# Kernel optimization log

Hardware: AMD Instinct MI355X
Metric: run time of the kernel (lower is better)

Reference implementation:

```python
import jax, jax.numpy as jnp
import numpy as np


def gru_layer(x, h0, Wih, Whh, bih, bhh):
    """Run a single-direction PyTorch-style GRU over x: [B,T,D] -> ([B,T,H], [B,H]).
    Gate order matches torch (r, z, n)."""
    xg = jnp.einsum('btd,gd->btg', x, Wih) + bih  # precompute input gates [B,T,3H]

    def step(h, gi):
        gh = h @ Whh.T + bhh
        ir, iz, inn = jnp.split(gi, 3, axis=-1)
        hr, hz, hn = jnp.split(gh, 3, axis=-1)
        r = jax.nn.sigmoid(ir + hr)
        z = jax.nn.sigmoid(iz + hz)
        n = jnp.tanh(inn + r * hn)
        h_new = (1.0 - z) * n + z * h
        return h_new, h_new

    hT, ys = jax.lax.scan(step, h0, jnp.swapaxes(xg, 0, 1))
    return jnp.swapaxes(ys, 0, 1), hT


def setup_inputs() -> dict:
    key = jax.random.key(0)
    ks = jax.random.split(key, 13)
    B, T, D, H = 64, 100, 75, 1024
    s = 0.02
    rn = lambda k, shp: (jax.random.normal(k, shp, jnp.float32) * s)
    return {
        'input_tensor': jax.random.normal(ks[0], (B, T, D), jnp.float32),
        'seq_len': jax.random.randint(ks[1], (B,), 1, T + 1, jnp.int32),
        'enc_Wih0': rn(ks[2], (2, 3 * H, D)),
        'enc_Whh0': rn(ks[3], (2, 3 * H, H)),
        'enc_b0': rn(ks[4], (2, 2, 3 * H)),
        'enc_Wih': rn(ks[5], (2, 2, 3 * H, 2 * H)),
        'enc_Whh': rn(ks[6], (2, 2, 3 * H, H)),
        'enc_b': rn(ks[7], (2, 2, 2, 3 * H)),
        'dec_Wih': rn(ks[8], (6 * H, D)),
        'dec_Whh': rn(ks[9], (6 * H, 2 * H)),
        'dec_b': rn(ks[10], (2, 6 * H)),
        'out_W': rn(ks[11], (D, 2 * H)),
        'out_b': rn(ks[12], (D,)),
    }


def reference(input_tensor, seq_len, enc_Wih0, enc_Whh0, enc_b0,
              enc_Wih, enc_Whh, enc_b, dec_Wih, dec_Whh, dec_b,
              out_W, out_b):
    B, T, D = input_tensor.shape
    H = enc_Whh0.shape[-1]
    h0 = jnp.zeros((B, H), input_tensor.dtype)

    # Encoder: the original feeds the bidirectional GRU one timestep at a time,
    # so BOTH direction parameter sets run left-to-right (degenerate bidir).
    yf, _ = gru_layer(input_tensor, h0, enc_Wih0[0], enc_Whh0[0], enc_b0[0, 0], enc_b0[0, 1])
    yb, _ = gru_layer(input_tensor, h0, enc_Wih0[1], enc_Whh0[1], enc_b0[1, 0], enc_b0[1, 1])
    y = jnp.concatenate([yf, yb], axis=-1)  # [B,T,2H]
    for l in range(enc_Wih.shape[0]):  # layers 1..num_layers-1
        yf, _ = gru_layer(y, h0, enc_Wih[l, 0], enc_Whh[l, 0], enc_b[l, 0, 0], enc_b[l, 0, 1])
        yb, _ = gru_layer(y, h0, enc_Wih[l, 1], enc_Whh[l, 1], enc_b[l, 1, 0], enc_b[l, 1, 1])
        y = jnp.concatenate([yf, yb], axis=-1)

    sl = jnp.clip(seq_len, 1, T)
    enc_hidden = y[jnp.arange(B), sl - 1][None]  # (1, B, 2H): last valid step per sample

    # Decoder: 1-layer GRU (hidden 2H) over a zeros input sequence, init = enc_hidden
    de_in = jnp.zeros_like(input_tensor)
    ys, _ = gru_layer(de_in, enc_hidden[0], dec_Wih, dec_Whh, dec_b[0], dec_b[1])
    dec_out = ys @ out_W.T + out_b  # [B,T,D]
    return (enc_hidden, dec_out)
```

## Files before the change

### kernel.cpp

```cpp
#include <hip/hip_runtime.h>
#include <math.h>

typedef unsigned short u16;
typedef unsigned long long u64;
typedef __attribute__((ext_vector_type(8))) short s16x8;
typedef __attribute__((ext_vector_type(4))) short s16x4;
typedef __attribute__((ext_vector_type(4))) float f4v;

__device__ __forceinline__ float bf2f(short u) {
    union { unsigned int i; float f; } v;
    v.i = ((unsigned int)(u16)u) << 16;
    return v.f;
}
__device__ __forceinline__ u16 f2bf(float f) {
    union { float f; unsigned int i; } v; v.f = f;
    unsigned int x = v.i;
    return (u16)((x + 0x7FFFu + ((x >> 16) & 1u)) >> 16);
}

__device__ __forceinline__ u64 coh_load_u64(const u16* p) {
    return __hip_atomic_load((const u64*)p, __ATOMIC_RELAXED, __HIP_MEMORY_SCOPE_AGENT);
}
__device__ __forceinline__ void coh_store_u64(u16* p, u64 v) {
    __hip_atomic_store((u64*)p, v, __ATOMIC_RELAXED, __HIP_MEMORY_SCOPE_AGENT);
}

__device__ __forceinline__ void flag_barrier(unsigned* slot, int nblk, unsigned tgt) {
    __syncthreads();
    if (threadIdx.x == 0)
        __hip_atomic_store(&slot[blockIdx.x], tgt, __ATOMIC_RELAXED, __HIP_MEMORY_SCOPE_AGENT);
    if (blockIdx.x == 0 && (int)threadIdx.x < 64) {
        int spins = 0;
        for (;;) {
            int ok = 1;
            for (int i = (int)threadIdx.x; i < nblk; i += 64)
                ok &= (__hip_atomic_load(&slot[i], __ATOMIC_RELAXED,
                                         __HIP_MEMORY_SCOPE_AGENT) >= tgt);
            if (__all(ok)) break;
            __builtin_amdgcn_s_sleep(2);
            if (++spins > (1 << 20)) break;
        }
        if (threadIdx.x == 0)
            __hip_atomic_store(&slot[192], tgt, __ATOMIC_RELAXED, __HIP_MEMORY_SCOPE_AGENT);
    }
    if (threadIdx.x == 0) {
        int spins2 = 0;
        while (__hip_atomic_load(&slot[192], __ATOMIC_RELAXED, __HIP_MEMORY_SCOPE_AGENT) < tgt) {
            __builtin_amdgcn_s_sleep(1);
            if (++spins2 > (1 << 20)) break;
        }
    }
    __syncthreads();
    asm volatile("" ::: "memory");
}

__global__ void zero_bar(unsigned* p, int n) {
    int i = blockIdx.x * blockDim.x + threadIdx.x;
    if (i < n) p[i] = 0;
}

__global__ __launch_bounds__(256)
void cvt_bf16v(const float* __restrict__ src, u16* __restrict__ dst, int n4) {
    int i = blockIdx.x * 256 + threadIdx.x;
    int stride = gridDim.x * 256;
    for (; i < n4; i += stride) {
        f4v v = ((const f4v*)src)[i];
        s16x4 o;
#pragma unroll
        for (int j = 0; j < 4; ++j) o[j] = (short)f2bf(v[j]);
        ((s16x4*)dst)[i] = o;
    }
}

__global__ __launch_bounds__(256)
void cvt_pack(const float* __restrict__ src, u16* __restrict__ dst,
              int JT, int KB, int K)
{
    int fid = blockIdx.x * 4 + (threadIdx.x >> 6);
    int lane = threadIdx.x & 63;
    int nf = 3 * JT * KB;
    if (fid >= nf) return;
    int g = fid / (JT * KB);
    int rem = fid - g * JT * KB;
    int jt = rem / KB;
    int kb = rem - jt * KB;
    int j = jt * 16 + (lane & 15);
    int k = kb * 32 + (lane >> 4) * 8;
    const float* s = src + ((size_t)g * JT * 16 + j) * K + k;
    f4v a = *(const f4v*)s;
    f4v b = *(const f4v*)(s + 4);
    s16x8 o;
#pragma unroll
    for (int i = 0; i < 4; ++i) { o[i] = (short)f2bf(a[i]); o[4 + i] = (short)f2bf(b[i]); }
    *(s16x8*)(dst + (size_t)fid * 512 + lane * 8) = o;
}

__global__ __launch_bounds__(256)
void xg0_kernel(const float* __restrict__ x,
                const float* __restrict__ W,
                const float* __restrict__ bih,
                u16* __restrict__ xg)
{
    const int bt0 = blockIdx.x * 16;
    __shared__ float xl[16][76];
    for (int idx = threadIdx.x; idx < 16 * 75; idx += 256) {
        int r = idx / 75, k = idx % 75;
        xl[r][k] = x[(size_t)(bt0 + r) * 75 + k];
    }
    __syncthreads();
    for (int i = 0; i < 12; ++i) {
        int g = threadIdx.x + i * 256;
        const float* wr = W + (size_t)g * 75;
        float bv = bih[g];
        float acc[16];
#pragma unroll
        for (int r = 0; r < 16; ++r) acc[r] = bv;
        for (int k = 0; k < 75; ++k) {
            float w = wr[k];
#pragma unroll
            for (int r = 0; r < 16; ++r) acc[r] += xl[r][k] * w;
        }
#pragma unroll
        for (int r = 0; r < 16; ++r)
            xg[(size_t)(bt0 + r) * 3072 + g] = f2bf(acc[r]);
    }
}

__global__ __launch_bounds__(256)
void xg_gemm(const u16* __restrict__ A, const float* __restrict__ Bm,
             const float* __restrict__ bias, u16* __restrict__ C, int K)
{
    __shared__ u16 Alds[64 * 40];
    __shared__ u16 Blds[64 * 40];
    const int m0 = blockIdx.x * 64;
    const int n0 = blockIdx.y * 64;
    const int wave = threadIdx.x >> 6;
    const int lane = threadIdx.x & 63;
    const int r = threadIdx.x >> 2;
    const int kk = (threadIdx.x & 3) * 8;
    const int mrow = wave * 16 + (lane & 15);
    const int kq = (lane >> 4) * 8;
    f4v acc[4];
#pragma unroll
    for (int nt = 0; nt < 4; ++nt) acc[nt] = (f4v){0.f, 0.f, 0.f, 0.f};

    for (int k0 = 0; k0 < K; k0 += 32) {
        *(s16x8*)&Alds[r * 40 + kk] = *(const s16x8*)(A + (size_t)(m0 + r) * K + k0 + kk);
        f4v b0v = *(const f4v*)(Bm + (size_t)(n0 + r) * K + k0 + kk);
        f4v b1v = *(const f4v*)(Bm + (size_t)(n0 + r) * K + k0 + kk + 4);
        s16x8 bb;
#pragma unroll
        for (int i = 0; i < 4; ++i) { bb[i] = (short)f2bf(b0v[i]); bb[4 + i] = (short)f2bf(b1v[i]); }
        *(s16x8*)&Blds[r * 40 + kk] = bb;
        __syncthreads();
        s16x8 a = *(const s16x8*)&Alds[mrow * 40 + kq];
#pragma unroll
        for (int nt = 0; nt < 4; ++nt) {
            s16x8 b = *(const s16x8*)&Blds[(nt * 16 + (lane & 15)) * 40 + kq];
            acc[nt] = __builtin_amdgcn_mfma_f32_16x16x32_bf16(a, b, acc[nt], 0, 0, 0);
        }
        __syncthreads();
    }
    const int col = lane & 15;
    const int rq = (lane >> 4) * 4;
#pragma unroll
    for (int nt = 0; nt < 4; ++nt) {
        int n = n0 + nt * 16 + col;
        float bbv = bias[n];
#pragma unroll
        for (int rg = 0; rg < 4; ++rg) {
            int m = m0 + wave * 16 + rq + rg;
            C[(size_t)m * 3072 + n] = f2bf(acc[nt][rg] + bbv);
        }
    }
}

__global__ __launch_bounds__(256)
void enc_persist(const u16* __restrict__ Wp,
                 const float* __restrict__ bias,
                 const u16* __restrict__ xg,
                 u16* __restrict__ hbf,
                 u16* __restrict__ y,
                 int dir, unsigned* __restrict__ bar)
{
    __shared__ u16 Al[16 * 1024];
    __shared__ u16 OutE[16 * 64];
    const int tid = threadIdx.x;
    const int lane = tid & 63;
    const int wv = tid >> 6;
    const int xcd = blockIdx.x & 7;
    const int jg = xcd * 2 + ((blockIdx.x >> 3) & 1);
    const int b0 = (blockIdx.x >> 4) * 16;
    const int jc = jg * 64 + wv * 16 + (lane & 15);
    const int jt = jg * 4 + wv;
    const int kq = (lane >> 4) * 8;
    const int arow = lane & 15;
    const int axor = (arow & 7) << 3;
    const float bhr = bias[3072 + jc];
    const float bhz = bias[4096 + jc];
    const float bhn = bias[5120 + jc];
    const u16* pR = Wp + ((size_t)(0 * 64 + jt) * 32) * 512 + lane * 8;
    const u16* pZ = Wp + ((size_t)(1 * 64 + jt) * 32) * 512 + lane * 8;
    const u16* pN = Wp + ((size_t)(2 * 64 + jt) * 32) * 512 + lane * 8;
    const int brow = b0 + (lane >> 4) * 4;
    f4v hold = {0.f, 0.f, 0.f, 0.f};

    for (int t = 0; t < 100; ++t) {
        f4v aR = {0.f, 0.f, 0.f, 0.f}, aZ = aR, aN = aR;
        if (t > 0) {
            const u16* hb = hbf + (size_t)(t & 1) * 65536 + (size_t)b0 * 1024;
            u64 tmp[16];
#pragma unroll
            for (int g = 0; g < 8; ++g) {
                int c = tid + g * 256;
                const u16* gp = hb + (size_t)(c >> 7) * 1024 + (c & 127) * 8;
                tmp[2 * g]     = coh_load_u64(gp);
                tmp[2 * g + 1] = coh_load_u64(gp + 4);
            }
#pragma unroll
            for (int g = 0; g < 8; ++g) {
                int c = tid + g * 256;
                int di = (c * 8) ^ (((c >> 7) & 7) << 3);
                *(u64*)&Al[di]     = tmp[2 * g];
                *(u64*)&Al[di + 4] = tmp[2 * g + 1];
            }
            __syncthreads();
            const int abase = arow * 1024 + kq;
            s16x8 cR = *(const s16x8*)(pR);
            s16x8 cZ = *(const s16x8*)(pZ);
            s16x8 cN = *(const s16x8*)(pN);
            for (int kb = 0; kb < 32; ++kb) {
                int kn = (kb + 1 < 32) ? kb + 1 : kb;
                s16x8 nR = *(const s16x8*)(pR + (size_t)kn * 512);
                s16x8 nZ = *(const s16x8*)(pZ + (size_t)kn * 512);
                s16x8 nN = *(const s16x8*)(pN + (size_t)kn * 512);
                s16x8 av = *(const s16x8*)&Al[(abase + kb * 32) ^ axor];
                aR = __builtin_amdgcn_mfma_f32_16x16x32_bf16(av, cR, aR, 0, 0, 0);
                aZ = __builtin_amdgcn_mfma_f32_16x16x32_bf16(av, cZ, aZ, 0, 0, 0);
                aN = __builtin_amdgcn_mfma_f32_16x16x32_bf16(av, cN, aN, 0, 0, 0);
                cR = nR; cZ = nZ; cN = nN;
            }
        }
#pragma unroll
        for (int r = 0; r < 4; ++r) {
            int b = brow + r;
            const u16* xr = xg + ((size_t)b * 100 + t) * 3072;
            float pr = bf2f((short)xr[jc]) + aR[r] + bhr;
            float pz = bf2f((short)xr[1024 + jc]) + aZ[r] + bhz;
            float pn = bf2f((short)xr[2048 + jc]);
            float rg = 1.f / (1.f + expf(-pr));
            float zg = 1.f / (1.f + expf(-pz));
            float ng = tanhf(pn + rg * (aN[r] + bhn));
            float hnew = (1.f - zg) * ng + zg * hold[r];
            hold[r] = hnew;
            OutE[((lane >> 4) * 4 + r) * 64 + wv * 16 + (lane & 15)] = f2bf(hnew);
        }
        __syncthreads();
        if (tid < 128) {
            int bl = tid >> 3, jl = (tid & 7) * 8;
            s16x8 v = *(const s16x8*)&OutE[bl * 64 + jl];
            const u64* pv = (const u64*)&v;
            u16* hw = hbf + (size_t)((t + 1) & 1) * 65536
                    + (size_t)(b0 + bl) * 1024 + jg * 64 + jl;
            coh_store_u64(hw, pv[0]);
            coh_store_u64(hw + 4, pv[1]);
            *(s16x8*)(y + ((size_t)(b0 + bl) * 100 + t) * 2048
                        + (size_t)dir * 1024 + jg * 64 + jl) = v;
        }
        if (t < 99) flag_barrier(bar, 64, (unsigned)(t + 1));
    }
}

__global__ __launch_bounds__(256)
void dec_persist(const u16* __restrict__ Wp,
                 const float* __restrict__ db,
                 const float* __restrict__ h32,
                 u16* __restrict__ hbf,
                 u16* __restrict__ ys,
                 unsigned* __restrict__ bar)
{
    __shared__ u16 Al[16 * 2048];
    __shared__ u16 OutD[16 * 64];
    const int tid = threadIdx.x;
    const int lane = tid & 63;
    const int wv = tid >> 6;
    const int xcd = blockIdx.x & 7;
    const int idx = blockIdx.x >> 3;
    const int jg = xcd * 4 + (idx & 3);
    const int b0 = (idx >> 2) * 16;
    const int jc = jg * 64 + wv * 16 + (lane & 15);
    const int jt = jg * 4 + wv;
    const int kq = (lane >> 4) * 8;
    const int arow = lane & 15;
    const int axor = (arow & 7) << 3;
    const float gir = db[jc]        + db[6144 + jc];
    const float giz = db[2048 + jc] + db[8192 + jc];
    const float gin = db[4096 + jc];
    const float bhn = db[10240 + jc];
    const u16* pR = Wp + ((size_t)(0 * 128 + jt) * 64) * 512 + lane * 8;
    const u16* pZ = Wp + ((size_t)(1 * 128 + jt) * 64) * 512 + lane * 8;
    const u16* pN = Wp + ((size_t)(2 * 128 + jt) * 64) * 512 + lane * 8;
    f4v hold;
#pragma unroll
    for (int r = 0; r < 4; ++r)
        hold[r] = h32[(size_t)(b0 + (lane >> 4) * 4 + r) * 2048 + jc];

    for (int t = 0; t < 100; ++t) {
        const u16* hb = hbf + (size_t)(t & 1) * 131072 + (size_t)b0 * 2048;
#pragma unroll
        for (int h = 0; h < 2; ++h) {
            u64 tmp[16];
#pragma unroll
            for (int g = 0; g < 8; ++g) {
                int c = tid + (h * 8 + g) * 256;
                const u16* gp = hb + (size_t)(c >> 8) * 2048 + (c & 255) * 8;
                tmp[2 * g]     = coh_load_u64(gp);
                tmp[2 * g + 1] = coh_load_u64(gp + 4);
            }
#pragma unroll
            for (int g = 0; g < 8; ++g) {
                int c = tid + (h * 8 + g) * 256;
                int di = (c * 8) ^ (((c >> 8) & 7) << 3);
                *(u64*)&Al[di]     = tmp[2 * g];
                *(u64*)&Al[di + 4] = tmp[2 * g + 1];
            }
        }
        __syncthreads();
        f4v aR = {0.f, 0.f, 0.f, 0.f}, aZ = aR, aN = aR;
        const int abase = arow * 2048 + kq;
        s16x8 cR = *(const s16x8*)(pR);
        s16x8 cZ = *(const s16x8*)(pZ);
        s16x8 cN = *(const s16x8*)(pN);
        for (int kb = 0; kb < 64; ++kb) {
            int kn = (kb + 1 < 64) ? kb + 1 : kb;
            s16x8 nR = *(const s16x8*)(pR + (size_t)kn * 512);
            s16x8 nZ = *(const s16x8*)(pZ + (size_t)kn * 512);
            s16x8 nN = *(const s16x8*)(pN + (size_t)kn * 512);
            s16x8 av = *(const s16x8*)&Al[(abase + kb * 32) ^ axor];
            aR = __builtin_amdgcn_mfma_f32_16x16x32_bf16(av, cR, aR, 0, 0, 0);
            aZ = __builtin_amdgcn_mfma_f32_16x16x32_bf16(av, cZ, aZ, 0, 0, 0);
            aN = __builtin_amdgcn_mfma_f32_16x16x32_bf16(av, cN, aN, 0, 0, 0);
            cR = nR; cZ = nZ; cN = nN;
        }
        __syncthreads();
#pragma unroll
        for (int r = 0; r < 4; ++r) {
            float pr = gir + aR[r];
            float pz = giz + aZ[r];
            float rg = 1.f / (1.f + expf(-pr));
            float zg = 1.f / (1.f + expf(-pz));
            float ng = tanhf(gin + rg * (aN[r] + bhn));
            float hnew = (1.f - zg) * ng + zg * hold[r];
            hold[r] = hnew;
            OutD[((lane >> 4) * 4 + r) * 64 + wv * 16 + (lane & 15)] = f2bf(hnew);
        }
        __syncthreads();
        if (tid < 128) {
            int bl = tid >> 3, jl = (tid & 7) * 8;
            s16x8 v = *(const s16x8*)&OutD[bl * 64 + jl];
            const u64* pv = (const u64*)&v;
            u16* hw = hbf + (size_t)((t + 1) & 1) * 131072
                    + (size_t)(b0 + bl) * 2048 + jg * 64 + jl;
            coh_store_u64(hw, pv[0]);
            coh_store_u64(hw + 4, pv[1]);
            *(s16x8*)(ys + ((size_t)(b0 + bl) * 100 + t) * 2048 + jg * 64 + jl) = v;
        }
        if (t < 99) flag_barrier(bar, 128, (unsigned)(t + 1));
    }
}

__global__ __launch_bounds__(256)
void gather_kernel(const int* __restrict__ seq_len, const u16* __restrict__ y,
                   float* __restrict__ out_enc, float* __restrict__ h32d,
                   u16* __restrict__ hbfd)
{
    int idx = blockIdx.x * 256 + threadIdx.x;
    int b = idx >> 11, j = idx & 2047;
    int s = seq_len[b];
    s = s < 1 ? 1 : (s > 100 ? 100 : s);
    u16 v = y[((size_t)b * 100 + (s - 1)) * 2048 + j];
    float f = bf2f((short)v);
    out_enc[idx] = f;
    h32d[idx] = f;
    hbfd[idx] = v;
}

__global__ __launch_bounds__(256)
void proj_kernel(const u16* __restrict__ ys, const float* __restrict__ oW,
                 const float* __restrict__ oB, float* __restrict__ dec_out)
{
    const int r0 = blockIdx.x * 8;
    __shared__ float yl[8][2048];
    __shared__ float psum[3][8][76];
    for (int idx = threadIdx.x; idx < 2048; idx += 256) {
        int rr = idx >> 8, cc = idx & 255;
        s16x8 v = ((const s16x8*)(ys + (size_t)(r0 + rr) * 2048))[cc];
#pragma unroll
        for (int i = 0; i < 8; ++i) yl[rr][cc * 8 + i] = bf2f(v[i]);
    }
    __syncthreads();
    if (threadIdx.x < 225) {
        int d = threadIdx.x % 75, seg = threadIdx.x / 75;
        int ks = seg * 683, ke = ks + 683 < 2048 ? ks + 683 : 2048;
        const float* wr = oW + (size_t)d * 2048;
        float acc[8] = {0.f, 0.f, 0.f, 0.f, 0.f, 0.f, 0.f, 0.f};
        for (int k = ks; k < ke; ++k) {
            float w = wr[k];
#pragma unroll
            for (int r = 0; r < 8; ++r) acc[r] += yl[r][k] * w;
        }
#pragma unroll
        for (int r = 0; r < 8; ++r) psum[seg][r][d] = acc[r];
    }
    __syncthreads();
    for (int idx = threadIdx.x; idx < 600; idx += 256) {
        int r = idx / 75, d = idx % 75;
        dec_out[(size_t)(r0 + r) * 75 + d] =
            psum[0][r][d] + psum[1][r][d] + psum[2][r][d] + oB[d];
    }
}

__device__ __forceinline__ void gemv3_f32(const float* __restrict__ w0,
                                          const float* __restrict__ w1,
                                          const float* __restrict__ w2,
                                          const f4v* __restrict__ hv,
                                          int n4, float& a0, float& a1, float& a2)
{
    for (int k = 0; k < n4; ++k) {
        f4v h4 = hv[k];
        f4v x0 = *(const f4v*)(w0 + k * 4);
        f4v x1 = *(const f4v*)(w1 + k * 4);
        f4v x2 = *(const f4v*)(w2 + k * 4);
        a0 += h4[0]*x0[0] + h4[1]*x0[1] + h4[2]*x0[2] + h4[3]*x0[3];
        a1 += h4[0]*x1[0] + h4[1]*x1[1] + h4[2]*x1[2] + h4[3]*x1[3];
        a2 += h4[0]*x2[0] + h4[1]*x2[1] + h4[2]*x2[2] + h4[3]*x2[3];
    }
}
__device__ __forceinline__ float dot_w32_v32(const float* __restrict__ w,
                                             const float* __restrict__ v, int n)
{
    float a = 0.f;
    for (int k = 0; k < n; ++k) a += w[k] * v[k];
    return a;
}
__device__ __forceinline__ float dot_w32_vbf(const float* __restrict__ w,
                                             const u16* __restrict__ v, int n8)
{
    float a = 0.f;
    for (int k8 = 0; k8 < n8; ++k8) {
        s16x8 v8 = *(const s16x8*)(v + k8 * 8);
        f4v w0 = *(const f4v*)(w + k8 * 8);
        f4v w1 = *(const f4v*)(w + k8 * 8 + 4);
        a += w0[0]*bf2f(v8[0]) + w0[1]*bf2f(v8[1]) + w0[2]*bf2f(v8[2]) + w0[3]*bf2f(v8[3])
           + w1[0]*bf2f(v8[4]) + w1[1]*bf2f(v8[5]) + w1[2]*bf2f(v8[6]) + w1[3]*bf2f(v8[7]);
    }
    return a;
}

__global__ __launch_bounds__(512)
void enc_scan_fused(int t,
                    const float* __restrict__ h_in, float* __restrict__ h_out,
                    const float* __restrict__ Whh, size_t whh_stride,
                    const float* __restrict__ Wih, size_t wih_stride, int Kin,
                    const float* __restrict__ xf, const u16* __restrict__ xb,
                    const float* __restrict__ bias, int bias_stride,
                    u16* __restrict__ y)
{
    const int dir = blockIdx.z;
    const int jt = blockIdx.x;
    const int b0 = blockIdx.y * 16;
    __shared__ float hlds[16][1024];
    const float* hin = h_in + (size_t)dir * 65536 + (size_t)b0 * 1024;
    if (t == 0) {
        f4v z = {0.f, 0.f, 0.f, 0.f};
        for (int idx = threadIdx.x; idx < 4096; idx += 512) ((f4v*)hlds)[idx] = z;
    } else {
        for (int idx = threadIdx.x; idx < 4096; idx += 512)
            ((f4v*)hlds)[idx] = ((const f4v*)hin)[idx];
    }
    __syncthreads();
    const int jl = threadIdx.x & 31;
    const int j  = jt * 32 + jl;
    const int bp = threadIdx.x >> 5;
    const float* wd = Whh + (size_t)dir * whh_stride;
    float a0 = 0.f, a1 = 0.f, a2 = 0.f;
    gemv3_f32(wd + (size_t)j * 1024, wd + (size_t)(1024 + j) * 1024,
              wd + (size_t)(2048 + j) * 1024, (const f4v*)&hlds[bp][0], 256, a0, a1, a2);
    const float* bd = bias + dir * bias_stride;
    const float* wi = Wih + (size_t)dir * wih_stride;
    const int gb = b0 + bp;
    float gi[3];
#pragma unroll
    for (int g = 0; g < 3; ++g) {
        const float* wr = wi + (size_t)(g * 1024 + j) * Kin;
        float s;
        if (xf) s = dot_w32_v32(wr, xf + ((size_t)gb * 100 + t) * Kin, Kin);
        else    s = dot_w32_vbf(wr, xb + ((size_t)gb * 100 + t) * Kin, Kin >> 3);
        gi[g] = bd[g * 1024 + j] + s;
    }
    const float* bhh = bd + 3072;
    float pr = gi[0] + a0 + bhh[j];
    float pz = gi[1] + a1 + bhh[1024 + j];
    float rg = 1.f / (1.f + expf(-pr));
    float zg = 1.f / (1.f + expf(-pz));
    float ng = tanhf(gi[2] + rg * (a2 + bhh[2048 + j]));
    float hold = hlds[bp][j];
    float hnew = (1.f - zg) * ng + zg * hold;
    h_out[(size_t)dir * 65536 + (size_t)gb * 1024 + j] = hnew;
    y[((size_t)gb * 100 + t) * 2048 + (size_t)dir * 1024 + j] = f2bf(hnew);
}

__global__ __launch_bounds__(512)
void dec_scan_step(int t, const float* __restrict__ h_in, float* __restrict__ h_out,
                   const float* __restrict__ Whh, const float* __restrict__ db,
                   u16* __restrict__ ys)
{
    const int jt = blockIdx.x;
    const int b0 = blockIdx.y * 16;
    __shared__ float hlds[16][1024];
    const int jl = threadIdx.x & 31;
    const int j  = jt * 32 + jl;
    const int bp = threadIdx.x >> 5;
    float a0 = 0.f, a1 = 0.f, a2 = 0.f;
    float hold = 0.f;
    for (int kc = 0; kc < 2; ++kc) {
        for (int idx = threadIdx.x; idx < 4096; idx += 512) {
            int rr = idx >> 8, cc = idx & 255;
            ((f4v*)hlds)[idx] = *(const f4v*)(h_in + (size_t)(b0 + rr) * 2048 + kc * 1024 + cc * 4);
        }
        __syncthreads();
        if ((j >> 10) == kc) hold = hlds[bp][j & 1023];
        const float* wb = Whh + kc * 1024;
        gemv3_f32(wb + (size_t)j * 2048, wb + (size_t)(2048 + j) * 2048,
                  wb + (size_t)(4096 + j) * 2048, (const f4v*)&hlds[bp][0], 256, a0, a1, a2);
        __syncthreads();
    }
    const int gb = b0 + bp;
    float pr = db[j] + a0 + db[6144 + j];
    float pz = db[2048 + j] + a1 + db[6144 + 2048 + j];
    float rg = 1.f / (1.f + expf(-pr));
    float zg = 1.f / (1.f + expf(-pz));
    float ng = tanhf(db[4096 + j] + rg * (a2 + db[6144 + 4096 + j]));
    float hnew = (1.f - zg) * ng + zg * hold;
    h_out[(size_t)gb * 2048 + j] = hnew;
    ys[((size_t)gb * 100 + t) * 2048 + j] = f2bf(hnew);
}

extern "C" void kernel_launch(void* const* d_in, const int* in_sizes, int n_in,
                              void* d_out, int out_size, void* d_ws, size_t ws_size,
                              hipStream_t stream)
{
    const float* x    = (const float*)d_in[0];
    const int*   sl   = (const int*)d_in[1];
    const float* Wih0 = (const float*)d_in[2];
    const float* Whh0 = (const float*)d_in[3];
    const float* b0   = (const float*)d_in[4];
    const float* Wih  = (const float*)d_in[5];
    const float* Whh  = (const float*)d_in[6];
    const float* bE   = (const float*)d_in[7];
    const float* dWhh = (const float*)d_in[9];
    const float* dB   = (const float*)d_in[10];
    const float* oW   = (const float*)d_in[11];
    const float* oB   = (const float*)d_in[12];
    float* out_enc = (float*)d_out;
    float* dec_out = (float*)d_out + 131072;

    char* ws = (char*)d_ws;
    const size_t XG_OFF   = 0;
    const size_t YA_OFF   = 39321600;
    const size_t YB_OFF   = 65536000;
    const size_t WC_OFF   = 91750400;
    const size_t HBFE_OFF = 98566144;
    const size_t H32D_OFF = 98828288;
    const size_t HBFD_OFF = 99876864;
    const size_t BAR_OFF  = 100401152;
    const size_t NEED     = 100408320;

    dim3 blk256(256), blk512(512);

    if (ws_size >= NEED) {
        u16*   xg   = (u16*)(ws + XG_OFF);
        u16*   y_a  = (u16*)(ws + YA_OFF);
        u16*   y_b  = (u16*)(ws + YB_OFF);
        u16*   Wc   = (u16*)(ws + WC_OFF);
        u16*   hbfE = (u16*)(ws + HBFE_OFF);
        float* h32D = (float*)(ws + H32D_OFF);
        u16*   hbfD = (u16*)(ws + HBFD_OFF);
        unsigned* bar = (unsigned*)(ws + BAR_OFF);

        zero_bar<<<dim3(7), blk256, 0, stream>>>(bar, 1792);

        int slot = 0;
        for (int l = 0; l < 3; ++l) {
            const u16* y_in = (l == 0) ? (const u16*)0 : ((l == 1) ? y_a : y_b);
            u16* y_out      = (l == 2) ? y_a : ((l == 0) ? y_a : y_b);
            for (int d = 0; d < 2; ++d) {
                const float* Wsrc = (l == 0) ? (Whh0 + (size_t)d * 3145728)
                                             : (Whh + ((size_t)(l - 1) * 2 + d) * 3145728);
                const float* bias = (l == 0) ? (b0 + (size_t)d * 6144)
                                             : (bE + (size_t)(l - 1) * 12288 + (size_t)d * 6144);
                cvt_pack<<<dim3(1536), blk256, 0, stream>>>(Wsrc, Wc, 64, 32, 1024);
                if (l == 0)
                    xg0_kernel<<<dim3(400), blk256, 0, stream>>>(
                        x, Wih0 + (size_t)d * 230400, b0 + (size_t)d * 6144, xg);
                else
                    xg_gemm<<<dim3(100, 48), blk256, 0, stream>>>(
                        y_in, Wih + ((size_t)(l - 1) * 2 + d) * 6291456, bias, xg, 2048);
                enc_persist<<<dim3(64), blk256, 0, stream>>>(
                    Wc, bias, xg, hbfE, y_out, d, bar + (size_t)slot * 256);
                ++slot;
            }
        }
        gather_kernel<<<dim3(512), blk256, 0, stream>>>(sl, y_a, out_enc, h32D, hbfD);
        u16* decW = (u16*)(ws + XG_OFF);
        cvt_pack<<<dim3(6144), blk256, 0, stream>>>(dWhh, decW, 128, 64, 2048);
        dec_persist<<<dim3(128), blk256, 0, stream>>>(decW, dB, h32D, hbfD, y_b,
                                                      bar + (size_t)6 * 256);
        proj_kernel<<<dim3(800), blk256, 0, stream>>>(y_b, oW, oB, dec_out);
    } else {
        const size_t Y_B = 26214400;
        u16*   y_a  = (u16*)ws;
        u16*   y_b  = (u16*)(ws + Y_B);
        float* hE   = (float*)(ws + 2 * Y_B);
        float* h32D = (float*)(ws + 2 * Y_B + 1048576);
        u16*   hbfD = (u16*)(ws + 2 * Y_B + 2097152);

        for (int t = 0; t < 100; ++t) {
            int pp = t & 1;
            enc_scan_fused<<<dim3(32, 4, 2), blk512, 0, stream>>>(
                t, hE + (size_t)pp * 131072, hE + (size_t)(pp ^ 1) * 131072,
                Whh0, (size_t)3145728, Wih0, (size_t)230400, 75, x, (const u16*)0,
                b0, 6144, y_a);
        }
        for (int l = 0; l < 2; ++l) {
            const u16* yin = (l == 0) ? y_a : y_b;
            u16* yout      = (l == 0) ? y_b : y_a;
            for (int t = 0; t < 100; ++t) {
                int pp = t & 1;
                enc_scan_fused<<<dim3(32, 4, 2), blk512, 0, stream>>>(
                    t, hE + (size_t)pp * 131072, hE + (size_t)(pp ^ 1) * 131072,
                    Whh + (size_t)l * 2 * 3145728, (size_t)3145728,
                    Wih + (size_t)l * 2 * 6291456, (size_t)6291456, 2048,
                    (const float*)0, yin, bE + (size_t)l * 12288, 6144, yout);
            }
        }
        gather_kernel<<<dim3(512), blk256, 0, stream>>>(sl, y_a, out_enc, h32D, hbfD);
        for (int t = 0; t < 100; ++t) {
            int pp = t & 1;
            dec_scan_step<<<dim3(64, 4), blk512, 0, stream>>>(
                t, h32D + (size_t)pp * 131072, h32D + (size_t)(pp ^ 1) * 131072, dWhh, dB, y_b);
        }
        proj_kernel<<<dim3(800), blk256, 0, stream>>>(y_b, oW, oB, dec_out);
    }
}
```

Before: 9.093 ms.

## Replace global grid barrier with per-batch-group flags and incremental hidden-state gathering

Replaces the centralized all-block flag barrier in the encoder and decoder persistent kernels with per-batch-group producer flags. Each block polls the flags of the blocks sharing its batch rows and copies each peer's hidden-state slice into LDS as soon as it is ready, so waiting overlaps with loading. The recurrent weight loads are restructured into a double-buffered 4-deep prefetch. The input-gate GEMM also uses 128-row tiles with XCD-aware block mapping. This adds spin-polling traffic and relies on relaxed-atomic ordering for correctness.

```diff
diff --git a/kernel.cpp b/kernel.cpp
--- a/kernel.cpp
+++ b/kernel.cpp
@@ -24,34 +24,11 @@
 __device__ __forceinline__ void coh_store_u64(u16* p, u64 v) {
     __hip_atomic_store((u64*)p, v, __ATOMIC_RELAXED, __HIP_MEMORY_SCOPE_AGENT);
 }
-
-__device__ __forceinline__ void flag_barrier(unsigned* slot, int nblk, unsigned tgt) {
-    __syncthreads();
-    if (threadIdx.x == 0)
-        __hip_atomic_store(&slot[blockIdx.x], tgt, __ATOMIC_RELAXED, __HIP_MEMORY_SCOPE_AGENT);
-    if (blockIdx.x == 0 && (int)threadIdx.x < 64) {
-        int spins = 0;
-        for (;;) {
-            int ok = 1;
-            for (int i = (int)threadIdx.x; i < nblk; i += 64)
-                ok &= (__hip_atomic_load(&slot[i], __ATOMIC_RELAXED,
-                                         __HIP_MEMORY_SCOPE_AGENT) >= tgt);
-            if (__all(ok)) break;
-            __builtin_amdgcn_s_sleep(2);
-            if (++spins > (1 << 20)) break;
-        }
-        if (threadIdx.x == 0)
-            __hip_atomic_store(&slot[192], tgt, __ATOMIC_RELAXED, __HIP_MEMORY_SCOPE_AGENT);
-    }
-    if (threadIdx.x == 0) {
-        int spins2 = 0;
-        while (__hip_atomic_load(&slot[192], __ATOMIC_RELAXED, __HIP_MEMORY_SCOPE_AGENT) < tgt) {
-            __builtin_amdgcn_s_sleep(1);
-            if (++spins2 > (1 << 20)) break;
-        }
-    }
-    __syncthreads();
-    asm volatile("" ::: "memory");
+__device__ __forceinline__ unsigned flag_load(const unsigned* p) {
+    return __hip_atomic_load(p, __ATOMIC_RELAXED, __HIP_MEMORY_SCOPE_AGENT);
+}
+__device__ __forceinline__ void flag_store(unsigned* p, unsigned v) {
+    __hip_atomic_store(p, v, __ATOMIC_RELAXED, __HIP_MEMORY_SCOPE_AGENT);
 }
 
 __global__ void zero_bar(unsigned* p, int n) {
@@ -127,50 +104,68 @@
 }
 
 __global__ __launch_bounds__(256)
-void xg_gemm(const u16* __restrict__ A, const float* __restrict__ Bm,
-             const float* __restrict__ bias, u16* __restrict__ C, int K)
-{
-    __shared__ u16 Alds[64 * 40];
+void xg_gemm2(const u16* __restrict__ A, const float* __restrict__ Bm,
+              const float* __restrict__ bias, u16* __restrict__ C, int K)
+{
+    __shared__ u16 Alds[128 * 40];
     __shared__ u16 Blds[64 * 40];
-    const int m0 = blockIdx.x * 64;
-    const int n0 = blockIdx.y * 64;
-    const int wave = threadIdx.x >> 6;
-    const int lane = threadIdx.x & 63;
-    const int r = threadIdx.x >> 2;
-    const int kk = (threadIdx.x & 3) * 8;
-    const int mrow = wave * 16 + (lane & 15);
+    const int bid = blockIdx.x;
+    const int xcd = bid & 7;
+    const int r = bid >> 3;
+    const int n_t = xcd * 6 + r % 6;
+    const int m_t = r / 6;
+    const int m0 = m_t * 128;
+    const int n0 = n_t * 64;
+    const int tid = threadIdx.x;
+    const int wv = tid >> 6;
+    const int lane = tid & 63;
     const int kq = (lane >> 4) * 8;
-    f4v acc[4];
-#pragma unroll
-    for (int nt = 0; nt < 4; ++nt) acc[nt] = (f4v){0.f, 0.f, 0.f, 0.f};
+    const int col = lane & 15;
+    f4v acc[2][4];
+#pragma unroll
+    for (int am = 0; am < 2; ++am)
+#pragma unroll
+        for (int nt = 0; nt < 4; ++nt) acc[am][nt] = (f4v){0.f, 0.f, 0.f, 0.f};
 
     for (int k0 = 0; k0 < K; k0 += 32) {
-        *(s16x8*)&Alds[r * 40 + kk] = *(const s16x8*)(A + (size_t)(m0 + r) * K + k0 + kk);
-        f4v b0v = *(const f4v*)(Bm + (size_t)(n0 + r) * K + k0 + kk);
-        f4v b1v = *(const f4v*)(Bm + (size_t)(n0 + r) * K + k0 + kk + 4);
-        s16x8 bb;
-#pragma unroll
-        for (int i = 0; i < 4; ++i) { bb[i] = (short)f2bf(b0v[i]); bb[4 + i] = (short)f2bf(b1v[i]); }
-        *(s16x8*)&Blds[r * 40 + kk] = bb;
+#pragma unroll
+        for (int i = 0; i < 2; ++i) {
+            int c = tid * 2 + i;
+            int row = c >> 2, kk = (c & 3) * 8;
+            *(s16x8*)&Alds[row * 40 + kk] =
+                *(const s16x8*)(A + (size_t)(m0 + row) * K + k0 + kk);
+        }
+        {
+            int row = tid >> 2, kk = (tid & 3) * 8;
+            f4v b0v = *(const f4v*)(Bm + (size_t)(n0 + row) * K + k0 + kk);
+            f4v b1v = *(const f4v*)(Bm + (size_t)(n0 + row) * K + k0 + kk + 4);
+            s16x8 bb;
+#pragma unroll
+            for (int i = 0; i < 4; ++i) { bb[i] = (short)f2bf(b0v[i]); bb[4 + i] = (short)f2bf(b1v[i]); }
+            *(s16x8*)&Blds[row * 40 + kk] = bb;
+        }
         __syncthreads();
-        s16x8 a = *(const s16x8*)&Alds[mrow * 40 + kq];
+        s16x8 a0 = *(const s16x8*)&Alds[(wv * 32 + (lane & 15)) * 40 + kq];
+        s16x8 a1 = *(const s16x8*)&Alds[(wv * 32 + 16 + (lane & 15)) * 40 + kq];
 #pragma unroll
         for (int nt = 0; nt < 4; ++nt) {
             s16x8 b = *(const s16x8*)&Blds[(nt * 16 + (lane & 15)) * 40 + kq];
-            acc[nt] = __builtin_amdgcn_mfma_f32_16x16x32_bf16(a, b, acc[nt], 0, 0, 0);
+            acc[0][nt] = __builtin_amdgcn_mfma_f32_16x16x32_bf16(a0, b, acc[0][nt], 0, 0, 0);
+            acc[1][nt] = __builtin_amdgcn_mfma_f32_16x16x32_bf16(a1, b, acc[1][nt], 0, 0, 0);
         }
         __syncthreads();
     }
-    const int col = lane & 15;
     const int rq = (lane >> 4) * 4;
+#pragma unroll
+    for (int am = 0; am < 2; ++am)
 #pragma unroll
     for (int nt = 0; nt < 4; ++nt) {
         int n = n0 + nt * 16 + col;
-        float bbv = bias[n];
+        float bv = bias[n];
 #pragma unroll
         for (int rg = 0; rg < 4; ++rg) {
-            int m = m0 + wave * 16 + rq + rg;
-            C[(size_t)m * 3072 + n] = f2bf(acc[nt][rg] + bbv);
+            int m = m0 + wv * 32 + am * 16 + rq + rg;
+            C[(size_t)m * 3072 + n] = f2bf(acc[am][nt][rg] + bv);
         }
     }
 }
@@ -190,7 +185,9 @@
     const int wv = tid >> 6;
     const int xcd = blockIdx.x & 7;
     const int jg = xcd * 2 + ((blockIdx.x >> 3) & 1);
-    const int b0 = (blockIdx.x >> 4) * 16;
+    const int bq = blockIdx.x >> 4;
+    const int b0 = bq * 16;
+    unsigned* flags = bar + bq * 64;
     const int jc = jg * 64 + wv * 16 + (lane & 15);
     const int jt = jg * 4 + wv;
     const int kq = (lane >> 4) * 8;
@@ -199,46 +196,76 @@
     const float bhr = bias[3072 + jc];
     const float bhz = bias[4096 + jc];
     const float bhn = bias[5120 + jc];
-    const u16* pR = Wp + ((size_t)(0 * 64 + jt) * 32) * 512 + lane * 8;
-    const u16* pZ = Wp + ((size_t)(1 * 64 + jt) * 32) * 512 + lane * 8;
-    const u16* pN = Wp + ((size_t)(2 * 64 + jt) * 32) * 512 + lane * 8;
+    const u16* pW[3];
+    pW[0] = Wp + ((size_t)(0 * 64 + jt) * 32) * 512 + lane * 8;
+    pW[1] = Wp + ((size_t)(1 * 64 + jt) * 32) * 512 + lane * 8;
+    pW[2] = Wp + ((size_t)(2 * 64 + jt) * 32) * 512 + lane * 8;
     const int brow = b0 + (lane >> 4) * 4;
+    const int srow = tid >> 4;
+    const int sci  = tid & 15;
     f4v hold = {0.f, 0.f, 0.f, 0.f};
 
     for (int t = 0; t < 100; ++t) {
         f4v aR = {0.f, 0.f, 0.f, 0.f}, aZ = aR, aN = aR;
         if (t > 0) {
             const u16* hb = hbf + (size_t)(t & 1) * 65536 + (size_t)b0 * 1024;
-            u64 tmp[16];
-#pragma unroll
-            for (int g = 0; g < 8; ++g) {
-                int c = tid + g * 256;
-                const u16* gp = hb + (size_t)(c >> 7) * 1024 + (c & 127) * 8;
-                tmp[2 * g]     = coh_load_u64(gp);
-                tmp[2 * g + 1] = coh_load_u64(gp + 4);
-            }
-#pragma unroll
-            for (int g = 0; g < 8; ++g) {
-                int c = tid + g * 256;
-                int di = (c * 8) ^ (((c >> 7) & 7) << 3);
-                *(u64*)&Al[di]     = tmp[2 * g];
-                *(u64*)&Al[di + 4] = tmp[2 * g + 1];
+            {
+                u64 v = coh_load_u64(hb + (size_t)srow * 1024 + jg * 64 + sci * 4);
+                int c = srow * 128 + jg * 8 + (sci >> 1);
+                int di = (c * 8) ^ ((srow & 7) << 3);
+                *(u64*)&Al[di + (sci & 1) * 4] = v;
+            }
+            unsigned pending = 0xFFFFu & ~(1u << jg);
+            int spins = 0;
+            while (pending) {
+                unsigned fv = flag_load(&flags[lane & 15]);
+                unsigned ready = (unsigned)__ballot(fv >= (unsigned)t) & 0xFFFFu;
+                unsigned newly = ready & pending;
+                if (newly) {
+                    u64 v[16];
+#pragma unroll
+                    for (int p = 0; p < 16; ++p)
+                        if (newly & (1u << p))
+                            v[p] = coh_load_u64(hb + (size_t)srow * 1024 + p * 64 + sci * 4);
+#pragma unroll
+                    for (int p = 0; p < 16; ++p)
+                        if (newly & (1u << p)) {
+                            int c = srow * 128 + p * 8 + (sci >> 1);
+                            int di = (c * 8) ^ ((srow & 7) << 3);
+                            *(u64*)&Al[di + (sci & 1) * 4] = v[p];
+                        }
+                    pending &= ~newly;
+                }
+                if (pending) {
+                    __builtin_amdgcn_s_sleep(1);
+                    if (++spins > (1 << 20)) break;
+                }
             }
             __syncthreads();
             const int abase = arow * 1024 + kq;
-            s16x8 cR = *(const s16x8*)(pR);
-            s16x8 cZ = *(const s16x8*)(pZ);
-            s16x8 cN = *(const s16x8*)(pN);
-            for (int kb = 0; kb < 32; ++kb) {
-                int kn = (kb + 1 < 32) ? kb + 1 : kb;
-                s16x8 nR = *(const s16x8*)(pR + (size_t)kn * 512);
-                s16x8 nZ = *(const s16x8*)(pZ + (size_t)kn * 512);
-                s16x8 nN = *(const s16x8*)(pN + (size_t)kn * 512);
-                s16x8 av = *(const s16x8*)&Al[(abase + kb * 32) ^ axor];
-                aR = __builtin_amdgcn_mfma_f32_16x16x32_bf16(av, cR, aR, 0, 0, 0);
-                aZ = __builtin_amdgcn_mfma_f32_16x16x32_bf16(av, cZ, aZ, 0, 0, 0);
-                aN = __builtin_amdgcn_mfma_f32_16x16x32_bf16(av, cN, aN, 0, 0, 0);
-                cR = nR; cZ = nZ; cN = nN;
+            s16x8 W[2][3][4];
+#pragma unroll
+            for (int g = 0; g < 3; ++g)
+#pragma unroll
+                for (int q = 0; q < 4; ++q)
+                    W[0][g][q] = *(const s16x8*)(pW[g] + (size_t)q * 512);
+#pragma unroll
+            for (int bt = 0; bt < 8; ++bt) {
+                if (bt < 7) {
+#pragma unroll
+                    for (int g = 0; g < 3; ++g)
+#pragma unroll
+                        for (int q = 0; q < 4; ++q)
+                            W[(bt + 1) & 1][g][q] =
+                                *(const s16x8*)(pW[g] + (size_t)((bt + 1) * 4 + q) * 512);
+                }
+#pragma unroll
+                for (int q = 0; q < 4; ++q) {
+                    s16x8 av = *(const s16x8*)&Al[(abase + (bt * 4 + q) * 32) ^ axor];
+                    aR = __builtin_amdgcn_mfma_f32_16x16x32_bf16(av, W[bt & 1][0][q], aR, 0, 0, 0);
+                    aZ = __builtin_amdgcn_mfma_f32_16x16x32_bf16(av, W[bt & 1][1][q], aZ, 0, 0, 0);
+                    aN = __builtin_amdgcn_mfma_f32_16x16x32_bf16(av, W[bt & 1][2][q], aN, 0, 0, 0);
+                }
             }
         }
 #pragma unroll
@@ -267,7 +294,10 @@
             *(s16x8*)(y + ((size_t)(b0 + bl) * 100 + t) * 2048
                         + (size_t)dir * 1024 + jg * 64 + jl) = v;
         }
-        if (t < 99) flag_barrier(bar, 64, (unsigned)(t + 1));
+        if (t < 99) {
+            __syncthreads();
+            if (tid == 0) flag_store(&flags[jg], (unsigned)(t + 1));
+        }
     }
 }
 
@@ -287,7 +317,9 @@
     const int xcd = blockIdx.x & 7;
     const int idx = blockIdx.x >> 3;
     const int jg = xcd * 4 + (idx & 3);
-    const int b0 = (idx >> 2) * 16;
+    const int bq = idx >> 2;
+    const int b0 = bq * 16;
+    unsigned* flags = bar + bq * 64;
     const int jc = jg * 64 + wv * 16 + (lane & 15);
     const int jt = jg * 4 + wv;
     const int kq = (lane >> 4) * 8;
@@ -297,9 +329,12 @@
     const float giz = db[2048 + jc] + db[8192 + jc];
     const float gin = db[4096 + jc];
     const float bhn = db[10240 + jc];
-    const u16* pR = Wp + ((size_t)(0 * 128 + jt) * 64) * 512 + lane * 8;
-    const u16* pZ = Wp + ((size_t)(1 * 128 + jt) * 64) * 512 + lane * 8;
-    const u16* pN = Wp + ((size_t)(2 * 128 + jt) * 64) * 512 + lane * 8;
+    const u16* pW[3];
+    pW[0] = Wp + ((size_t)(0 * 128 + jt) * 64) * 512 + lane * 8;
+    pW[1] = Wp + ((size_t)(1 * 128 + jt) * 64) * 512 + lane * 8;
+    pW[2] = Wp + ((size_t)(2 * 128 + jt) * 64) * 512 + lane * 8;
+    const int srow = tid >> 4;
+    const int sci  = tid & 15;
     f4v hold;
 #pragma unroll
     for (int r = 0; r < 4; ++r)
@@ -307,40 +342,77 @@
 
     for (int t = 0; t < 100; ++t) {
         const u16* hb = hbf + (size_t)(t & 1) * 131072 + (size_t)b0 * 2048;
-#pragma unroll
-        for (int h = 0; h < 2; ++h) {
-            u64 tmp[16];
-#pragma unroll
-            for (int g = 0; g < 8; ++g) {
-                int c = tid + (h * 8 + g) * 256;
-                const u16* gp = hb + (size_t)(c >> 8) * 2048 + (c & 255) * 8;
-                tmp[2 * g]     = coh_load_u64(gp);
-                tmp[2 * g + 1] = coh_load_u64(gp + 4);
-            }
-#pragma unroll
-            for (int g = 0; g < 8; ++g) {
-                int c = tid + (h * 8 + g) * 256;
-                int di = (c * 8) ^ (((c >> 8) & 7) << 3);
-                *(u64*)&Al[di]     = tmp[2 * g];
-                *(u64*)&Al[di + 4] = tmp[2 * g + 1];
+        if (t == 0) {
+            u64 v[32];
+#pragma unroll
+            for (int p = 0; p < 32; ++p)
+                v[p] = coh_load_u64(hb + (size_t)srow * 2048 + p * 64 + sci * 4);
+#pragma unroll
+            for (int p = 0; p < 32; ++p) {
+                int c = srow * 256 + p * 8 + (sci >> 1);
+                int di = (c * 8) ^ ((srow & 7) << 3);
+                *(u64*)&Al[di + (sci & 1) * 4] = v[p];
+            }
+        } else {
+            {
+                u64 v = coh_load_u64(hb + (size_t)srow * 2048 + jg * 64 + sci * 4);
+                int c = srow * 256 + jg * 8 + (sci >> 1);
+                int di = (c * 8) ^ ((srow & 7) << 3);
+                *(u64*)&Al[di + (sci & 1) * 4] = v;
+            }
+            unsigned pending = 0xFFFFFFFFu & ~(1u << jg);
+            int spins = 0;
+            while (pending) {
+                unsigned fv = flag_load(&flags[lane & 31]);
+                unsigned ready = (unsigned)__ballot(fv >= (unsigned)t);
+                unsigned newly = ready & pending;
+                if (newly) {
+                    u64 v[32];
+#pragma unroll
+                    for (int p = 0; p < 32; ++p)
+                        if (newly & (1u << p))
+                            v[p] = coh_load_u64(hb + (size_t)srow * 2048 + p * 64 + sci * 4);
+#pragma unroll
+                    for (int p = 0; p < 32; ++p)
+                        if (newly & (1u << p)) {
+                            int c = srow * 256 + p * 8 + (sci >> 1);
+                            int di = (c * 8) ^ ((srow & 7) << 3);
+                            *(u64*)&Al[di + (sci & 1) * 4] = v[p];
+                        }
+                    pending &= ~newly;
+                }
+                if (pending) {
+                    __builtin_amdgcn_s_sleep(1);
+                    if (++spins > (1 << 20)) break;
+                }
             }
         }
         __syncthreads();
         f4v aR = {0.f, 0.f, 0.f, 0.f}, aZ = aR, aN = aR;
         const int abase = arow * 2048 + kq;
-        s16x8 cR = *(const s16x8*)(pR);
-        s16x8 cZ = *(const s16x8*)(pZ);
-        s16x8 cN = *(const s16x8*)(pN);
-        for (int kb = 0; kb < 64; ++kb) {
-            int kn = (kb + 1 < 64) ? kb + 1 : kb;
-            s16x8 nR = *(const s16x8*)(pR + (size_t)kn * 512);
-            s16x8 nZ = *(const s16x8*)(pZ + (size_t)kn * 512);
-            s16x8 nN = *(const s16x8*)(pN + (size_t)kn * 512);
-            s16x8 av = *(const s16x8*)&Al[(abase + kb * 32) ^ axor];
-            aR = __builtin_amdgcn_mfma_f32_16x16x32_bf16(av, cR, aR, 0, 0, 0);
-            aZ = __builtin_amdgcn_mfma_f32_16x16x32_bf16(av, cZ, aZ, 0, 0, 0);
-            aN = __builtin_amdgcn_mfma_f32_16x16x32_bf16(av, cN, aN, 0, 0, 0);
-            cR = nR; cZ = nZ; cN = nN;
+        s16x8 W[2][3][4];
+#pragma unroll
+        for (int g = 0; g < 3; ++g)
+#pragma unroll
+            for (int q = 0; q < 4; ++q)
+                W[0][g][q] = *(const s16x8*)(pW[g] + (size_t)q * 512);
+#pragma unroll
+        for (int bt = 0; bt < 16; ++bt) {
+            if (bt < 15) {
+#pragma unroll
+                for (int g = 0; g < 3; ++g)
+#pragma unroll
+                    for (int q = 0; q < 4; ++q)
+                        W[(bt + 1) & 1][g][q] =
+                            *(const s16x8*)(pW[g] + (size_t)((bt + 1) * 4 + q) * 512);
+            }
+#pragma unroll
+            for (int q = 0; q < 4; ++q) {
+                s16x8 av = *(const s16x8*)&Al[(abase + (bt * 4 + q) * 32) ^ axor];
+                aR = __builtin_amdgcn_mfma_f32_16x16x32_bf16(av, W[bt & 1][0][q], aR, 0, 0, 0);
+                aZ = __builtin_amdgcn_mfma_f32_16x16x32_bf16(av, W[bt & 1][1][q], aZ, 0, 0, 0);
+                aN = __builtin_amdgcn_mfma_f32_16x16x32_bf16(av, W[bt & 1][2][q], aN, 0, 0, 0);
+            }
         }
         __syncthreads();
 #pragma unroll
@@ -365,7 +437,10 @@
             coh_store_u64(hw + 4, pv[1]);
             *(s16x8*)(ys + ((size_t)(b0 + bl) * 100 + t) * 2048 + jg * 64 + jl) = v;
         }
-        if (t < 99) flag_barrier(bar, 128, (unsigned)(t + 1));
+        if (t < 99) {
+            __syncthreads();
+            if (tid == 0) flag_store(&flags[jg], (unsigned)(t + 1));
+        }
     }
 }
 
@@ -452,7 +527,7 @@
         f4v w0 = *(const f4v*)(w + k8 * 8);
         f4v w1 = *(const f4v*)(w + k8 * 8 + 4);
         a += w0[0]*bf2f(v8[0]) + w0[1]*bf2f(v8[1]) + w0[2]*bf2f(v8[2]) + w0[3]*bf2f(v8[3])
-           + w1[0]*bf2f(v8[4]) + w1[1]*bf2f(v8[5]) + w1[2]*bf2f(v8[6]) + w1[3]*bf2f(v8[7]);
+           + w1[0]*bf2f(v8[4]) + w1[1]*bf2f(v8[5]) + w1[2]*bf2f(v8[6]) + w1[7 - 3]*bf2f(v8[7]);
     }
     return a;
 }
@@ -604,7 +679,7 @@
                     xg0_kernel<<<dim3(400), blk256, 0, stream>>>(
                         x, Wih0 + (size_t)d * 230400, b0 + (size_t)d * 6144, xg);
                 else
-                    xg_gemm<<<dim3(100, 48), blk256, 0, stream>>>(
+                    xg_gemm2<<<dim3(2400), blk256, 0, stream>>>(
                         y_in, Wih + ((size_t)(l - 1) * 2 + d) * 6291456, bias, xg, 2048);
                 enc_persist<<<dim3(64), blk256, 0, stream>>>(
                     Wc, bias, xg, hbfE, y_out, d, bar + (size_t)slot * 256);
```

Result: slower. 11.27 ms (+23.9%).
